# Kernel optimization log

Hardware: AMD Instinct MI355X
Metric: run time of the kernel (lower is better)

The kernel has to match this reference:

```python
import jax, jax.numpy as jnp
import numpy as np

N_HEAD = 16
N_EMBD = 64  # per-head dim in this module's convention
INNER = N_HEAD * N_EMBD  # 1024


def setup_inputs() -> dict:
    key = jax.random.key(0)
    ks = jax.random.split(key, 6)
    B, S = 4, 2048
    scale = 0.02
    return {
        "x": jax.random.normal(ks[0], (B, S, N_EMBD), dtype=jnp.float32),
        "Wq": jax.random.normal(ks[1], (N_EMBD, INNER), dtype=jnp.float32) * scale,
        "Wk": jax.random.normal(ks[2], (N_EMBD, INNER), dtype=jnp.float32) * scale,
        "Wv": jax.random.normal(ks[3], (N_EMBD, INNER), dtype=jnp.float32) * scale,
        "Wo": jax.random.normal(ks[4], (INNER, N_EMBD), dtype=jnp.float32) * scale,
        "bo": jax.random.normal(ks[5], (N_EMBD,), dtype=jnp.float32) * scale,
        "causal_mask": 1,
    }


def reference(x, Wq, Wk, Wv, Wo, bo, causal_mask):
    B, S, _ = x.shape
    # projections: [B,S,INNER] -> [B,H,S,D]
    def split_heads(t):
        return t.reshape(B, S, N_HEAD, N_EMBD).transpose(0, 2, 1, 3)
    q = split_heads(x @ Wq)
    k = split_heads(x @ Wk)
    v = split_heads(x @ Wv)
    # [B,H,S,S]
    scores = jnp.einsum("bhqd,bhkd->bhqk", q, k) / jnp.sqrt(jnp.float32(N_EMBD))
    if causal_mask:
        future = jnp.triu(jnp.ones((S, S), dtype=scores.dtype), k=1)
        scores = scores - 1e9 * future  # matches torch: subtract 1e9*mask
    attn = jax.nn.softmax(scores, axis=-1)
    out = jnp.einsum("bhqk,bhkd->bhqd", attn, v)
    out = out.transpose(0, 2, 1, 3).reshape(B, S, INNER)
    return out @ Wo + bo
```

## Files before the change

### kernel.cpp

```cpp
#include <hip/hip_runtime.h>
#include <hip/hip_bf16.h>

#define NHEAD 16
#define HDIM 64
#define DINNER 1024
#define NBATCH 4
#define SEQ 2048
#define NTOK (NBATCH*SEQ)

typedef __bf16 bf16;
typedef __bf16 bf16x4 __attribute__((ext_vector_type(4)));
typedef __bf16 bf16x8 __attribute__((ext_vector_type(8)));
typedef float f32x4 __attribute__((ext_vector_type(4)));

#define OFF_BO   8
#define OFF_XB   128
#define OFF_WQT  (OFF_XB + NTOK*HDIM)
#define OFF_WKT  (OFF_WQT + DINNER*HDIM)
#define OFF_WVT  (OFF_WKT + DINNER*HDIM)
#define OFF_WOT  (OFF_WVT + DINNER*HDIM)
#define OFF_Q    (OFF_WOT + DINNER*HDIM)
#define OFF_K    (OFF_Q + NTOK*DINNER)
#define OFF_VT   (OFF_K + NTOK*DINNER)
#define OFF_ATT  (OFF_VT + NTOK*DINNER)

#define SSCALE 0.18033688011112042f

static __device__ __forceinline__ bf16x8 ld8(const bf16* p) {
  return *reinterpret_cast<const bf16x8*>(p);
}

static __device__ __forceinline__ int detect_isbf(const void* x, int tid,
                                                  int* sflag) {
  if (tid < 64) {
    const unsigned short* xb = (const unsigned short*)x;
    bool ok = true;
#pragma unroll
    for (int i = 0; i < 8; i++) {
      unsigned e = (xb[tid * 8 + i] >> 7) & 0xFF;
      ok = ok && (e >= 64 && e <= 140);
    }
    unsigned long long mball = __ballot(ok);
    if (tid == 0) *sflag = (mball == ~0ull) ? 1 : 0;
  }
  __syncthreads();
  return *sflag;
}

__global__ __launch_bounds__(256) void prep_kernel(
    const void* __restrict__ x, const void* __restrict__ Wq,
    const void* __restrict__ Wk, const void* __restrict__ Wv,
    const void* __restrict__ Wo, const void* __restrict__ bo,
    bf16* __restrict__ ws) {
  __shared__ int sflag;
  int isbf = detect_isbf(x, threadIdx.x, &sflag);
  int z = blockIdx.y;
  int idx = blockIdx.x * 256 + threadIdx.x;
  if (z < 3) {
    const void* src = (z == 0) ? Wq : (z == 1) ? Wk : Wv;
    bf16* dst = ws + ((z == 0) ? OFF_WQT : (z == 1) ? OFF_WKT : OFF_WVT);
    int d = idx >> 10, n = idx & 1023;
    float v = isbf ? (float)((const bf16*)src)[idx] : ((const float*)src)[idx];
    if (z == 0) v *= SSCALE;
    dst[n * HDIM + d] = (bf16)v;
  } else if (z == 3) {
    int k = idx >> 6, n = idx & 63;
    float v = isbf ? (float)((const bf16*)Wo)[idx] : ((const float*)Wo)[idx];
    ws[OFF_WOT + n * DINNER + k] = (bf16)v;
  } else if (z == 4) {
    int i = idx * 8;
    bf16x8 v;
    if (isbf) {
      v = ld8((const bf16*)x + i);
    } else {
      f32x4 a = *reinterpret_cast<const f32x4*>((const float*)x + i);
      f32x4 b2 = *reinterpret_cast<const f32x4*>((const float*)x + i + 4);
#pragma unroll
      for (int j = 0; j < 4; j++) { v[j] = (bf16)a[j]; v[4 + j] = (bf16)b2[j]; }
    }
    *reinterpret_cast<bf16x8*>(&ws[OFF_XB + i]) = v;
  } else {
    if (idx < 64) ws[OFF_BO + idx] = isbf ? ((const bf16*)bo)[idx] : (bf16)((const float*)bo)[idx];
  }
}

__global__ __launch_bounds__(256) void qkv_kernel(bf16* __restrict__ ws) {
  __shared__ __align__(16) bf16 Vst[4][16 * 72];
  int tt = blockIdx.x, pz = blockIdx.z;
  int w = threadIdx.x >> 6;
  int nc = blockIdx.y * 4 + w;
  int lane = threadIdx.x & 63;
  int lq = lane & 15, quad = lane >> 4;
  const bf16* WT = ws + OFF_WQT + pz * (DINNER * HDIM);
  int n0 = nc * 64;
  bf16x8 w0[4], w1[4];
#pragma unroll
  for (int c = 0; c < 4; c++) {
    const bf16* wr = WT + (n0 + c * 16 + lq) * HDIM;
    w0[c] = ld8(wr + quad * 8);
    w1[c] = ld8(wr + 32 + quad * 8);
  }
  bf16* Qb = ws + OFF_Q;
  bf16* Kb = ws + OFF_K;
  bf16* VTb = ws + OFF_VT;
  bf16x8 ao0[4], ao1[4];
  if (pz == 2) {
    const bf16* WoT = ws + OFF_WOT;
#pragma unroll
    for (int c = 0; c < 4; c++) {
      const bf16* orow = WoT + (size_t)(c * 16 + lq) * DINNER + nc * 64;
      ao0[c] = ld8(orow + quad * 8);
      ao1[c] = ld8(orow + 32 + quad * 8);
    }
  }
#pragma unroll
  for (int mi = 0; mi < 4; mi++) {
    int t0 = tt * 64 + mi * 16;
    const bf16* xrow = ws + OFF_XB + (t0 + lq) * HDIM;
    bf16x8 x0 = ld8(xrow + quad * 8);
    bf16x8 x1 = ld8(xrow + 32 + quad * 8);
    int b = t0 >> 11, s0 = t0 & (SEQ - 1);
    if (pz < 2) {
#pragma unroll
      for (int c = 0; c < 4; c++) {
        f32x4 z = {0.f, 0.f, 0.f, 0.f};
        z = __builtin_amdgcn_mfma_f32_16x16x32_bf16(w0[c], x0, z, 0, 0, 0);
        z = __builtin_amdgcn_mfma_f32_16x16x32_bf16(w1[c], x1, z, 0, 0, 0);
        bf16x4 pk = {(bf16)z[0], (bf16)z[1], (bf16)z[2], (bf16)z[3]};
        bf16* P = (pz == 0) ? Qb : Kb;
        *reinterpret_cast<bf16x4*>(
            &P[((size_t)(b * NHEAD + nc) * SEQ + s0 + lq) * HDIM + c * 16 + quad * 4]) = pk;
      }
    } else {
#pragma unroll
      for (int c = 0; c < 4; c++) {
        f32x4 z = {0.f, 0.f, 0.f, 0.f};
        z = __builtin_amdgcn_mfma_f32_16x16x32_bf16(w0[c], x0, z, 0, 0, 0);
        z = __builtin_amdgcn_mfma_f32_16x16x32_bf16(w1[c], x1, z, 0, 0, 0);
        bf16x4 pk = {(bf16)z[0], (bf16)z[1], (bf16)z[2], (bf16)z[3]};
        *reinterpret_cast<bf16x4*>(&Vst[w][lq * 72 + c * 16 + quad * 4]) = pk;
      }
      bf16x8 bv0 = ld8(&Vst[w][lq * 72 + quad * 8]);
      bf16x8 bv1 = ld8(&Vst[w][lq * 72 + 32 + quad * 8]);
#pragma unroll
      for (int c = 0; c < 4; c++) {
        f32x4 z2 = {0.f, 0.f, 0.f, 0.f};
        z2 = __builtin_amdgcn_mfma_f32_16x16x32_bf16(ao0[c], bv0, z2, 0, 0, 0);
        z2 = __builtin_amdgcn_mfma_f32_16x16x32_bf16(ao1[c], bv1, z2, 0, 0, 0);
#pragma unroll
        for (int r = 0; r < 4; r++) {
          int d = c * 16 + quad * 4 + r;
          VTb[(((size_t)b * NHEAD + nc) * HDIM + d) * SEQ + s0 + lq] = (bf16)z2[r];
        }
      }
    }
  }
}

__global__ __launch_bounds__(256, 2) void flash_kernel(const int* __restrict__ cmask,
                                                       bf16* __restrict__ ws) {
  __shared__ __align__(16) bf16 Kl[2][64 * 64];
  __shared__ __align__(16) bf16 Vl[2][64 * 64];
  __shared__ __align__(16) bf16 Pl[4][16 * 64];
  const int qmap[16] = {15,13,11,9,0,2,4,6,14,12,10,8,1,3,5,7};
  int bid = blockIdx.x;
  int bh = (bid & 7) * 8 + ((bid >> 3) & 7);
  int qt = qmap[bid >> 6];
  int w = threadIdx.x >> 6;
  int lane = threadIdx.x & 63;
  int lq = lane & 15, quad = lane >> 4;
  int causal = cmask[0];
  const bf16* Q = ws + OFF_Q + (size_t)bh * SEQ * HDIM;
  const bf16* K = ws + OFF_K + (size_t)bh * SEQ * HDIM;
  const bf16* VT = ws + OFF_VT + (size_t)bh * HDIM * SEQ;
  int b = bh >> 4, h = bh & 15;
  bf16* ar = ws + OFF_ATT;
  int sr = threadIdx.x >> 2;
  int sg = (threadIdx.x & 3) * 16;
  int sc0 = (((threadIdx.x & 3) * 2) ^ (sr & 7)) << 3;
  int sc1 = (((threadIdx.x & 3) * 2 + 1) ^ (sr & 7)) << 3;
  int rq0 = (quad ^ (lq & 7)) << 3;
  int rq1 = ((4 + quad) ^ (lq & 7)) << 3;

  int qb = qt * 128;
  int qw = qb + w * 32;
  int T = (causal ? (qb + 128) : SEQ) / 64;

  bf16x8 bq[2][2];
#pragma unroll
  for (int m = 0; m < 2; m++) {
    const bf16* qrow = Q + (qw + m * 16 + lq) * HDIM;
    bq[m][0] = ld8(qrow + quad * 8);
    bq[m][1] = ld8(qrow + 32 + quad * 8);
  }
  f32x4 o[2][4];
  float lsum[2] = {0.f, 0.f};
#pragma unroll
  for (int m = 0; m < 2; m++)
#pragma unroll
    for (int c = 0; c < 4; c++) o[m][c] = (f32x4){0.f, 0.f, 0.f, 0.f};

  bf16x8 kst0 = ld8(K + sr * HDIM + sg);
  bf16x8 kst1 = ld8(K + sr * HDIM + sg + 8);
  bf16x8 vst0 = ld8(VT + sr * SEQ + sg);
  bf16x8 vst1 = ld8(VT + sr * SEQ + sg + 8);

  for (int ti = 0; ti < T; ti++) {
    int buf = ti & 1;
    int k0 = ti * 64;
    *reinterpret_cast<bf16x8*>(&Kl[buf][sr * 64 + sc0]) = kst0;
    *reinterpret_cast<bf16x8*>(&Kl[buf][sr * 64 + sc1]) = kst1;
    *reinterpret_cast<bf16x8*>(&Vl[buf][sr * 64 + sc0]) = vst0;
    *reinterpret_cast<bf16x8*>(&Vl[buf][sr * 64 + sc1]) = vst1;
    int kn = (ti + 1 < T) ? (k0 + 64) : k0;
    kst0 = ld8(K + (kn + sr) * HDIM + sg);
    kst1 = ld8(K + (kn + sr) * HDIM + sg + 8);
    vst0 = ld8(VT + sr * SEQ + kn + sg);
    vst1 = ld8(VT + sr * SEQ + kn + sg + 8);
    __syncthreads();
    f32x4 st[2][4];
#pragma unroll
    for (int t = 0; t < 4; t++) {
      bf16x8 a0 = ld8(&Kl[buf][(t * 16 + lq) * 64 + rq0]);
      bf16x8 a1 = ld8(&Kl[buf][(t * 16 + lq) * 64 + rq1]);
#pragma unroll
      for (int m = 0; m < 2; m++) {
        f32x4 z = {0.f, 0.f, 0.f, 0.f};
        z = __builtin_amdgcn_mfma_f32_16x16x32_bf16(a0, bq[m][0], z, 0, 0, 0);
        z = __builtin_amdgcn_mfma_f32_16x16x32_bf16(a1, bq[m][1], z, 0, 0, 0);
        st[m][t] = z;
      }
    }
    bool needmask = causal && (k0 + 63 > qw);
    bf16x8 bp[2][2];
#pragma unroll
    for (int m = 0; m < 2; m++) {
      if (needmask) {
        int qrel = qw + m * 16 + lq - k0 - quad * 4;
#pragma unroll
        for (int t = 0; t < 4; t++)
#pragma unroll
          for (int r = 0; r < 4; r++)
            if (t * 16 + r > qrel) st[m][t][r] = -200.0f;
      }
      float sum = 0.f;
#pragma unroll
      for (int t = 0; t < 4; t++) {
        float e0 = exp2f(st[m][t][0]);
        float e1 = exp2f(st[m][t][1]);
        float e2 = exp2f(st[m][t][2]);
        float e3 = exp2f(st[m][t][3]);
        sum += (e0 + e1) + (e2 + e3);
        bf16x4 pk = {(bf16)e0, (bf16)e1, (bf16)e2, (bf16)e3};
        int ch = ((t * 2 + (quad >> 1)) ^ (lq & 7)) << 3;
        *reinterpret_cast<bf16x4*>(&Pl[w][lq * 64 + ch + (quad & 1) * 4]) = pk;
      }
      lsum[m] += sum;
      bp[m][0] = ld8(&Pl[w][lq * 64 + rq0]);
      bp[m][1] = ld8(&Pl[w][lq * 64 + rq1]);
    }
#pragma unroll
    for (int c = 0; c < 4; c++) {
      bf16x8 av0 = ld8(&Vl[buf][(c * 16 + lq) * 64 + rq0]);
      bf16x8 av1 = ld8(&Vl[buf][(c * 16 + lq) * 64 + rq1]);
#pragma unroll
      for (int m = 0; m < 2; m++) {
        o[m][c] = __builtin_amdgcn_mfma_f32_16x16x32_bf16(av0, bp[m][0], o[m][c], 0, 0, 0);
        o[m][c] = __builtin_amdgcn_mfma_f32_16x16x32_bf16(av1, bp[m][1], o[m][c], 0, 0, 0);
      }
    }
  }
#pragma unroll
  for (int m = 0; m < 2; m++) {
    lsum[m] += __shfl_xor(lsum[m], 16);
    lsum[m] += __shfl_xor(lsum[m], 32);
    float inv = 1.0f / lsum[m];
    size_t rowoff = ((size_t)(b * SEQ + qw + m * 16 + lq)) * DINNER + h * HDIM;
#pragma unroll
    for (int c = 0; c < 4; c++) {
      bf16x4 ov = {(bf16)(o[m][c][0] * inv), (bf16)(o[m][c][1] * inv),
                   (bf16)(o[m][c][2] * inv), (bf16)(o[m][c][3] * inv)};
      *reinterpret_cast<bf16x4*>(&ar[rowoff + c * 16 + quad * 4]) = ov;
    }
  }
}

__global__ __launch_bounds__(256) void reduce_kernel(const bf16* __restrict__ ws,
                                                     const void* __restrict__ x,
                                                     void* __restrict__ outp) {
  __shared__ int sflag;
  int isbf = detect_isbf(x, threadIdx.x, &sflag);
  int idx = blockIdx.x * 256 + threadIdx.x;
  int t = idx >> 6, d = idx & 63;
  const bf16* ar = ws + OFF_ATT + (size_t)t * DINNER + d;
  float s = (float)ws[OFF_BO + d];
#pragma unroll
  for (int h = 0; h < 16; h++) s += (float)ar[h * 64];
  if (isbf) ((bf16*)outp)[idx] = (bf16)s;
  else      ((float*)outp)[idx] = s;
}

extern "C" void kernel_launch(void* const* d_in, const int* in_sizes, int n_in,
                              void* d_out, int out_size, void* d_ws, size_t ws_size,
                              hipStream_t stream) {
  const void* x  = d_in[0];
  const void* Wq = d_in[1];
  const void* Wk = d_in[2];
  const void* Wv = d_in[3];
  const void* Wo = d_in[4];
  const void* bo = d_in[5];
  const int* cm  = (const int*)d_in[6];
  bf16* ws = (bf16*)d_ws;

  hipLaunchKernelGGL(prep_kernel, dim3(256, 6), dim3(256), 0, stream,
                     x, Wq, Wk, Wv, Wo, bo, ws);
  hipLaunchKernelGGL(qkv_kernel, dim3(128, 4, 3), dim3(256), 0, stream, ws);
  hipLaunchKernelGGL(flash_kernel, dim3(1024), dim3(256), 0, stream, cm, ws);
  hipLaunchKernelGGL(reduce_kernel, dim3(2048), dim3(256), 0, stream, ws, x, d_out);
}
```

Measured before the change: 161.2 us.

## Fold input prep into QKV kernel and fuse head reduction into flash tail

Removes the separate prep kernel: the QKV kernel now reads and converts x and the weights directly from the inputs, with strided scalar loads for the transposed weight tiles. It also removes the reduce kernel: each flash block bumps an atomic counter per (batch, q-tile), and the last of the 16 head blocks sums the per-head outputs plus bias and writes the final result. This saves two launches and a workspace round trip, at the cost of uncoalesced weight loads repeated across every QKV block and a serialized tail in the last-arriving flash block. Correctness depends on the counters being zeroed by the QKV kernel before flash runs.

```diff
diff --git a/kernel.cpp b/kernel.cpp
--- a/kernel.cpp
+++ b/kernel.cpp
@@ -13,13 +13,7 @@
 typedef __bf16 bf16x8 __attribute__((ext_vector_type(8)));
 typedef float f32x4 __attribute__((ext_vector_type(4)));
 
-#define OFF_BO   8
-#define OFF_XB   128
-#define OFF_WQT  (OFF_XB + NTOK*HDIM)
-#define OFF_WKT  (OFF_WQT + DINNER*HDIM)
-#define OFF_WVT  (OFF_WKT + DINNER*HDIM)
-#define OFF_WOT  (OFF_WVT + DINNER*HDIM)
-#define OFF_Q    (OFF_WOT + DINNER*HDIM)
+#define OFF_Q    128
 #define OFF_K    (OFF_Q + NTOK*DINNER)
 #define OFF_VT   (OFF_K + NTOK*DINNER)
 #define OFF_ATT  (OFF_VT + NTOK*DINNER)
@@ -28,6 +22,9 @@
 
 static __device__ __forceinline__ bf16x8 ld8(const bf16* p) {
   return *reinterpret_cast<const bf16x8*>(p);
+}
+static __device__ __forceinline__ float ldw(const void* W, int i, int isbf) {
+  return isbf ? (float)((const bf16*)W)[i] : ((const float*)W)[i];
 }
 
 static __device__ __forceinline__ int detect_isbf(const void* x, int tid,
@@ -47,78 +44,71 @@
   return *sflag;
 }
 
-__global__ __launch_bounds__(256) void prep_kernel(
+__global__ __launch_bounds__(256) void qkv_kernel(
     const void* __restrict__ x, const void* __restrict__ Wq,
     const void* __restrict__ Wk, const void* __restrict__ Wv,
-    const void* __restrict__ Wo, const void* __restrict__ bo,
-    bf16* __restrict__ ws) {
+    const void* __restrict__ Wo, bf16* __restrict__ ws) {
+  __shared__ __align__(16) bf16 Vst[4][16 * 72];
   __shared__ int sflag;
   int isbf = detect_isbf(x, threadIdx.x, &sflag);
-  int z = blockIdx.y;
-  int idx = blockIdx.x * 256 + threadIdx.x;
-  if (z < 3) {
-    const void* src = (z == 0) ? Wq : (z == 1) ? Wk : Wv;
-    bf16* dst = ws + ((z == 0) ? OFF_WQT : (z == 1) ? OFF_WKT : OFF_WVT);
-    int d = idx >> 10, n = idx & 1023;
-    float v = isbf ? (float)((const bf16*)src)[idx] : ((const float*)src)[idx];
-    if (z == 0) v *= SSCALE;
-    dst[n * HDIM + d] = (bf16)v;
-  } else if (z == 3) {
-    int k = idx >> 6, n = idx & 63;
-    float v = isbf ? (float)((const bf16*)Wo)[idx] : ((const float*)Wo)[idx];
-    ws[OFF_WOT + n * DINNER + k] = (bf16)v;
-  } else if (z == 4) {
-    int i = idx * 8;
-    bf16x8 v;
-    if (isbf) {
-      v = ld8((const bf16*)x + i);
-    } else {
-      f32x4 a = *reinterpret_cast<const f32x4*>((const float*)x + i);
-      f32x4 b2 = *reinterpret_cast<const f32x4*>((const float*)x + i + 4);
-#pragma unroll
-      for (int j = 0; j < 4; j++) { v[j] = (bf16)a[j]; v[4 + j] = (bf16)b2[j]; }
-    }
-    *reinterpret_cast<bf16x8*>(&ws[OFF_XB + i]) = v;
-  } else {
-    if (idx < 64) ws[OFF_BO + idx] = isbf ? ((const bf16*)bo)[idx] : (bf16)((const float*)bo)[idx];
-  }
-}
-
-__global__ __launch_bounds__(256) void qkv_kernel(bf16* __restrict__ ws) {
-  __shared__ __align__(16) bf16 Vst[4][16 * 72];
   int tt = blockIdx.x, pz = blockIdx.z;
   int w = threadIdx.x >> 6;
   int nc = blockIdx.y * 4 + w;
   int lane = threadIdx.x & 63;
   int lq = lane & 15, quad = lane >> 4;
-  const bf16* WT = ws + OFF_WQT + pz * (DINNER * HDIM);
+  if (tt == 0 && pz == 0 && blockIdx.y == 0 && threadIdx.x < 64)
+    ((int*)ws)[threadIdx.x] = 0;
+  const void* W = (pz == 0) ? Wq : (pz == 1) ? Wk : Wv;
   int n0 = nc * 64;
   bf16x8 w0[4], w1[4];
 #pragma unroll
   for (int c = 0; c < 4; c++) {
-    const bf16* wr = WT + (n0 + c * 16 + lq) * HDIM;
-    w0[c] = ld8(wr + quad * 8);
-    w1[c] = ld8(wr + 32 + quad * 8);
+    int n = n0 + c * 16 + lq;
+#pragma unroll
+    for (int j = 0; j < 8; j++) {
+      float vA = ldw(W, (quad * 8 + j) * DINNER + n, isbf);
+      float vB = ldw(W, (32 + quad * 8 + j) * DINNER + n, isbf);
+      if (pz == 0) { vA *= SSCALE; vB *= SSCALE; }
+      w0[c][j] = (bf16)vA;
+      w1[c][j] = (bf16)vB;
+    }
+  }
+  bf16x8 ao0[4], ao1[4];
+  if (pz == 2) {
+#pragma unroll
+    for (int c = 0; c < 4; c++) {
+      int dout = c * 16 + lq;
+#pragma unroll
+      for (int j = 0; j < 8; j++) {
+        ao0[c][j] = (bf16)ldw(Wo, (n0 + quad * 8 + j) * HDIM + dout, isbf);
+        ao1[c][j] = (bf16)ldw(Wo, (n0 + 32 + quad * 8 + j) * HDIM + dout, isbf);
+      }
+    }
   }
   bf16* Qb = ws + OFF_Q;
   bf16* Kb = ws + OFF_K;
   bf16* VTb = ws + OFF_VT;
-  bf16x8 ao0[4], ao1[4];
-  if (pz == 2) {
-    const bf16* WoT = ws + OFF_WOT;
-#pragma unroll
-    for (int c = 0; c < 4; c++) {
-      const bf16* orow = WoT + (size_t)(c * 16 + lq) * DINNER + nc * 64;
-      ao0[c] = ld8(orow + quad * 8);
-      ao1[c] = ld8(orow + 32 + quad * 8);
-    }
-  }
 #pragma unroll
   for (int mi = 0; mi < 4; mi++) {
     int t0 = tt * 64 + mi * 16;
-    const bf16* xrow = ws + OFF_XB + (t0 + lq) * HDIM;
-    bf16x8 x0 = ld8(xrow + quad * 8);
-    bf16x8 x1 = ld8(xrow + 32 + quad * 8);
+    int trow = t0 + lq;
+    bf16x8 x0, x1;
+    if (isbf) {
+      const bf16* xr = (const bf16*)x + (size_t)trow * HDIM;
+      x0 = ld8(xr + quad * 8);
+      x1 = ld8(xr + 32 + quad * 8);
+    } else {
+      const float* xf = (const float*)x + (size_t)trow * HDIM;
+      f32x4 a0 = *reinterpret_cast<const f32x4*>(xf + quad * 8);
+      f32x4 a1 = *reinterpret_cast<const f32x4*>(xf + quad * 8 + 4);
+      f32x4 b0 = *reinterpret_cast<const f32x4*>(xf + 32 + quad * 8);
+      f32x4 b1 = *reinterpret_cast<const f32x4*>(xf + 32 + quad * 8 + 4);
+#pragma unroll
+      for (int j = 0; j < 4; j++) {
+        x0[j] = (bf16)a0[j]; x0[4 + j] = (bf16)a1[j];
+        x1[j] = (bf16)b0[j]; x1[4 + j] = (bf16)b1[j];
+      }
+    }
     int b = t0 >> 11, s0 = t0 & (SEQ - 1);
     if (pz < 2) {
 #pragma unroll
@@ -157,12 +147,17 @@
   }
 }
 
-__global__ __launch_bounds__(256, 2) void flash_kernel(const int* __restrict__ cmask,
-                                                       bf16* __restrict__ ws) {
+__global__ __launch_bounds__(256, 2) void flash_kernel(
+    const int* __restrict__ cmask, bf16* __restrict__ ws,
+    const void* __restrict__ x, const void* __restrict__ bo,
+    void* __restrict__ outp) {
   __shared__ __align__(16) bf16 Kl[2][64 * 64];
   __shared__ __align__(16) bf16 Vl[2][64 * 64];
   __shared__ __align__(16) bf16 Pl[4][16 * 64];
+  __shared__ int sflag;
+  __shared__ int isLast;
   const int qmap[16] = {15,13,11,9,0,2,4,6,14,12,10,8,1,3,5,7};
+  int isbf = detect_isbf(x, threadIdx.x, &sflag);
   int bid = blockIdx.x;
   int bh = (bid & 7) * 8 + ((bid >> 3) & 7);
   int qt = qmap[bid >> 6];
@@ -283,21 +278,27 @@
       *reinterpret_cast<bf16x4*>(&ar[rowoff + c * 16 + quad * 4]) = ov;
     }
   }
-}
-
-__global__ __launch_bounds__(256) void reduce_kernel(const bf16* __restrict__ ws,
-                                                     const void* __restrict__ x,
-                                                     void* __restrict__ outp) {
-  __shared__ int sflag;
-  int isbf = detect_isbf(x, threadIdx.x, &sflag);
-  int idx = blockIdx.x * 256 + threadIdx.x;
-  int t = idx >> 6, d = idx & 63;
-  const bf16* ar = ws + OFF_ATT + (size_t)t * DINNER + d;
-  float s = (float)ws[OFF_BO + d];
-#pragma unroll
-  for (int h = 0; h < 16; h++) s += (float)ar[h * 64];
-  if (isbf) ((bf16*)outp)[idx] = (bf16)s;
-  else      ((float*)outp)[idx] = s;
+  __threadfence();
+  if (threadIdx.x == 0) {
+    int old = atomicAdd(&((int*)ws)[b * 16 + qt], 1);
+    isLast = (old == 15);
+  }
+  __syncthreads();
+  if (isLast) {
+    __threadfence();
+#pragma unroll
+    for (int k = 0; k < 32; k++) {
+      int i = k * 256 + threadIdx.x;
+      int t = qb + (i >> 6), d = i & 63;
+      const bf16* arow = ws + OFF_ATT + ((size_t)(b * SEQ + t)) * DINNER + d;
+      float s = ldw(bo, d, isbf);
+#pragma unroll
+      for (int hh = 0; hh < 16; hh++) s += (float)arow[hh * 64];
+      size_t oo = (size_t)(b * SEQ + t) * HDIM + d;
+      if (isbf) ((bf16*)outp)[oo] = (bf16)s;
+      else      ((float*)outp)[oo] = s;
+    }
+  }
 }
 
 extern "C" void kernel_launch(void* const* d_in, const int* in_sizes, int n_in,
@@ -312,9 +313,8 @@
   const int* cm  = (const int*)d_in[6];
   bf16* ws = (bf16*)d_ws;
 
-  hipLaunchKernelGGL(prep_kernel, dim3(256, 6), dim3(256), 0, stream,
-                     x, Wq, Wk, Wv, Wo, bo, ws);
-  hipLaunchKernelGGL(qkv_kernel, dim3(128, 4, 3), dim3(256), 0, stream, ws);
-  hipLaunchKernelGGL(flash_kernel, dim3(1024), dim3(256), 0, stream, cm, ws);
-  hipLaunchKernelGGL(reduce_kernel, dim3(2048), dim3(256), 0, stream, ws, x, d_out);
-}
+  hipLaunchKernelGGL(qkv_kernel, dim3(128, 4, 3), dim3(256), 0, stream,
+                     x, Wq, Wk, Wv, Wo, ws);
+  hipLaunchKernelGGL(flash_kernel, dim3(1024), dim3(256), 0, stream,
+                     cm, ws, x, bo, d_out);
+}
```

Measured after the change: 320.1 us. 1.99x slower.

## Fuse Q/K/V projections into one block and read x directly

Applied to the files above, without the earlier changes.

The QKV projection kernel now computes Q, K and V (plus the Wo-folded V transform) in a single block, so each x tile is loaded once, where before each of three blocks loaded it. The bf16 staging copy of x in the prep kernel is removed and x is converted in registers inside the projection kernel, which also runs dtype detection. This cuts global traffic and one grid dimension, but raises per-thread register use from holding all four weight fragment sets at once, which may lower occupancy.

```diff
diff --git a/kernel.cpp b/kernel.cpp
--- a/kernel.cpp
+++ b/kernel.cpp
@@ -14,8 +14,7 @@
 typedef float f32x4 __attribute__((ext_vector_type(4)));
 
 #define OFF_BO   8
-#define OFF_XB   128
-#define OFF_WQT  (OFF_XB + NTOK*HDIM)
+#define OFF_WQT  128
 #define OFF_WKT  (OFF_WQT + DINNER*HDIM)
 #define OFF_WVT  (OFF_WKT + DINNER*HDIM)
 #define OFF_WOT  (OFF_WVT + DINNER*HDIM)
@@ -28,6 +27,9 @@
 
 static __device__ __forceinline__ bf16x8 ld8(const bf16* p) {
   return *reinterpret_cast<const bf16x8*>(p);
+}
+static __device__ __forceinline__ float ldw(const void* W, int i, int isbf) {
+  return isbf ? (float)((const bf16*)W)[i] : ((const float*)W)[i];
 }
 
 static __device__ __forceinline__ int detect_isbf(const void* x, int tid,
@@ -60,98 +62,99 @@
     const void* src = (z == 0) ? Wq : (z == 1) ? Wk : Wv;
     bf16* dst = ws + ((z == 0) ? OFF_WQT : (z == 1) ? OFF_WKT : OFF_WVT);
     int d = idx >> 10, n = idx & 1023;
-    float v = isbf ? (float)((const bf16*)src)[idx] : ((const float*)src)[idx];
+    float v = ldw(src, idx, isbf);
     if (z == 0) v *= SSCALE;
     dst[n * HDIM + d] = (bf16)v;
   } else if (z == 3) {
     int k = idx >> 6, n = idx & 63;
-    float v = isbf ? (float)((const bf16*)Wo)[idx] : ((const float*)Wo)[idx];
-    ws[OFF_WOT + n * DINNER + k] = (bf16)v;
-  } else if (z == 4) {
-    int i = idx * 8;
-    bf16x8 v;
-    if (isbf) {
-      v = ld8((const bf16*)x + i);
-    } else {
-      f32x4 a = *reinterpret_cast<const f32x4*>((const float*)x + i);
-      f32x4 b2 = *reinterpret_cast<const f32x4*>((const float*)x + i + 4);
-#pragma unroll
-      for (int j = 0; j < 4; j++) { v[j] = (bf16)a[j]; v[4 + j] = (bf16)b2[j]; }
-    }
-    *reinterpret_cast<bf16x8*>(&ws[OFF_XB + i]) = v;
+    ws[OFF_WOT + n * DINNER + k] = (bf16)ldw(Wo, idx, isbf);
   } else {
-    if (idx < 64) ws[OFF_BO + idx] = isbf ? ((const bf16*)bo)[idx] : (bf16)((const float*)bo)[idx];
-  }
-}
-
-__global__ __launch_bounds__(256) void qkv_kernel(bf16* __restrict__ ws) {
+    if (idx < 64) ws[OFF_BO + idx] = (bf16)ldw(bo, idx, isbf);
+  }
+}
+
+__global__ __launch_bounds__(256) void qkv_kernel(const void* __restrict__ x,
+                                                  bf16* __restrict__ ws) {
   __shared__ __align__(16) bf16 Vst[4][16 * 72];
-  int tt = blockIdx.x, pz = blockIdx.z;
+  __shared__ int sflag;
+  int isbf = detect_isbf(x, threadIdx.x, &sflag);
+  int tt = blockIdx.x;
   int w = threadIdx.x >> 6;
   int nc = blockIdx.y * 4 + w;
   int lane = threadIdx.x & 63;
   int lq = lane & 15, quad = lane >> 4;
-  const bf16* WT = ws + OFF_WQT + pz * (DINNER * HDIM);
   int n0 = nc * 64;
-  bf16x8 w0[4], w1[4];
+  bf16x8 wq0[4], wq1[4], wk0[4], wk1[4], wv0[4], wv1[4], ao0[4], ao1[4];
 #pragma unroll
   for (int c = 0; c < 4; c++) {
-    const bf16* wr = WT + (n0 + c * 16 + lq) * HDIM;
-    w0[c] = ld8(wr + quad * 8);
-    w1[c] = ld8(wr + 32 + quad * 8);
+    int n = n0 + c * 16 + lq;
+    const bf16* r;
+    r = ws + OFF_WQT + n * HDIM; wq0[c] = ld8(r + quad * 8); wq1[c] = ld8(r + 32 + quad * 8);
+    r = ws + OFF_WKT + n * HDIM; wk0[c] = ld8(r + quad * 8); wk1[c] = ld8(r + 32 + quad * 8);
+    r = ws + OFF_WVT + n * HDIM; wv0[c] = ld8(r + quad * 8); wv1[c] = ld8(r + 32 + quad * 8);
+    const bf16* orow = ws + OFF_WOT + (size_t)(c * 16 + lq) * DINNER + n0;
+    ao0[c] = ld8(orow + quad * 8); ao1[c] = ld8(orow + 32 + quad * 8);
   }
   bf16* Qb = ws + OFF_Q;
   bf16* Kb = ws + OFF_K;
   bf16* VTb = ws + OFF_VT;
-  bf16x8 ao0[4], ao1[4];
-  if (pz == 2) {
-    const bf16* WoT = ws + OFF_WOT;
-#pragma unroll
-    for (int c = 0; c < 4; c++) {
-      const bf16* orow = WoT + (size_t)(c * 16 + lq) * DINNER + nc * 64;
-      ao0[c] = ld8(orow + quad * 8);
-      ao1[c] = ld8(orow + 32 + quad * 8);
-    }
-  }
 #pragma unroll
   for (int mi = 0; mi < 4; mi++) {
     int t0 = tt * 64 + mi * 16;
-    const bf16* xrow = ws + OFF_XB + (t0 + lq) * HDIM;
-    bf16x8 x0 = ld8(xrow + quad * 8);
-    bf16x8 x1 = ld8(xrow + 32 + quad * 8);
+    bf16x8 x0, x1;
+    if (isbf) {
+      const bf16* xr = (const bf16*)x + (size_t)(t0 + lq) * HDIM;
+      x0 = ld8(xr + quad * 8);
+      x1 = ld8(xr + 32 + quad * 8);
+    } else {
+      const float* xf = (const float*)x + (size_t)(t0 + lq) * HDIM;
+      f32x4 a0 = *reinterpret_cast<const f32x4*>(xf + quad * 8);
+      f32x4 a1 = *reinterpret_cast<const f32x4*>(xf + quad * 8 + 4);
+      f32x4 b0 = *reinterpret_cast<const f32x4*>(xf + 32 + quad * 8);
+      f32x4 b1 = *reinterpret_cast<const f32x4*>(xf + 32 + quad * 8 + 4);
+#pragma unroll
+      for (int j = 0; j < 4; j++) {
+        x0[j] = (bf16)a0[j]; x0[4 + j] = (bf16)a1[j];
+        x1[j] = (bf16)b0[j]; x1[4 + j] = (bf16)b1[j];
+      }
+    }
     int b = t0 >> 11, s0 = t0 & (SEQ - 1);
-    if (pz < 2) {
-#pragma unroll
-      for (int c = 0; c < 4; c++) {
-        f32x4 z = {0.f, 0.f, 0.f, 0.f};
-        z = __builtin_amdgcn_mfma_f32_16x16x32_bf16(w0[c], x0, z, 0, 0, 0);
-        z = __builtin_amdgcn_mfma_f32_16x16x32_bf16(w1[c], x1, z, 0, 0, 0);
-        bf16x4 pk = {(bf16)z[0], (bf16)z[1], (bf16)z[2], (bf16)z[3]};
-        bf16* P = (pz == 0) ? Qb : Kb;
-        *reinterpret_cast<bf16x4*>(
-            &P[((size_t)(b * NHEAD + nc) * SEQ + s0 + lq) * HDIM + c * 16 + quad * 4]) = pk;
-      }
-    } else {
-#pragma unroll
-      for (int c = 0; c < 4; c++) {
-        f32x4 z = {0.f, 0.f, 0.f, 0.f};
-        z = __builtin_amdgcn_mfma_f32_16x16x32_bf16(w0[c], x0, z, 0, 0, 0);
-        z = __builtin_amdgcn_mfma_f32_16x16x32_bf16(w1[c], x1, z, 0, 0, 0);
-        bf16x4 pk = {(bf16)z[0], (bf16)z[1], (bf16)z[2], (bf16)z[3]};
-        *reinterpret_cast<bf16x4*>(&Vst[w][lq * 72 + c * 16 + quad * 4]) = pk;
-      }
-      bf16x8 bv0 = ld8(&Vst[w][lq * 72 + quad * 8]);
-      bf16x8 bv1 = ld8(&Vst[w][lq * 72 + 32 + quad * 8]);
-#pragma unroll
-      for (int c = 0; c < 4; c++) {
-        f32x4 z2 = {0.f, 0.f, 0.f, 0.f};
-        z2 = __builtin_amdgcn_mfma_f32_16x16x32_bf16(ao0[c], bv0, z2, 0, 0, 0);
-        z2 = __builtin_amdgcn_mfma_f32_16x16x32_bf16(ao1[c], bv1, z2, 0, 0, 0);
-#pragma unroll
-        for (int r = 0; r < 4; r++) {
-          int d = c * 16 + quad * 4 + r;
-          VTb[(((size_t)b * NHEAD + nc) * HDIM + d) * SEQ + s0 + lq] = (bf16)z2[r];
-        }
+    size_t rowbase = ((size_t)(b * NHEAD + nc) * SEQ + s0 + lq) * HDIM;
+#pragma unroll
+    for (int c = 0; c < 4; c++) {
+      f32x4 z = {0.f, 0.f, 0.f, 0.f};
+      z = __builtin_amdgcn_mfma_f32_16x16x32_bf16(wq0[c], x0, z, 0, 0, 0);
+      z = __builtin_amdgcn_mfma_f32_16x16x32_bf16(wq1[c], x1, z, 0, 0, 0);
+      bf16x4 pk = {(bf16)z[0], (bf16)z[1], (bf16)z[2], (bf16)z[3]};
+      *reinterpret_cast<bf16x4*>(&Qb[rowbase + c * 16 + quad * 4]) = pk;
+    }
+#pragma unroll
+    for (int c = 0; c < 4; c++) {
+      f32x4 z = {0.f, 0.f, 0.f, 0.f};
+      z = __builtin_amdgcn_mfma_f32_16x16x32_bf16(wk0[c], x0, z, 0, 0, 0);
+      z = __builtin_amdgcn_mfma_f32_16x16x32_bf16(wk1[c], x1, z, 0, 0, 0);
+      bf16x4 pk = {(bf16)z[0], (bf16)z[1], (bf16)z[2], (bf16)z[3]};
+      *reinterpret_cast<bf16x4*>(&Kb[rowbase + c * 16 + quad * 4]) = pk;
+    }
+#pragma unroll
+    for (int c = 0; c < 4; c++) {
+      f32x4 z = {0.f, 0.f, 0.f, 0.f};
+      z = __builtin_amdgcn_mfma_f32_16x16x32_bf16(wv0[c], x0, z, 0, 0, 0);
+      z = __builtin_amdgcn_mfma_f32_16x16x32_bf16(wv1[c], x1, z, 0, 0, 0);
+      bf16x4 pk = {(bf16)z[0], (bf16)z[1], (bf16)z[2], (bf16)z[3]};
+      *reinterpret_cast<bf16x4*>(&Vst[w][lq * 72 + c * 16 + quad * 4]) = pk;
+    }
+    bf16x8 bv0 = ld8(&Vst[w][lq * 72 + quad * 8]);
+    bf16x8 bv1 = ld8(&Vst[w][lq * 72 + 32 + quad * 8]);
+#pragma unroll
+    for (int c = 0; c < 4; c++) {
+      f32x4 z2 = {0.f, 0.f, 0.f, 0.f};
+      z2 = __builtin_amdgcn_mfma_f32_16x16x32_bf16(ao0[c], bv0, z2, 0, 0, 0);
+      z2 = __builtin_amdgcn_mfma_f32_16x16x32_bf16(ao1[c], bv1, z2, 0, 0, 0);
+#pragma unroll
+      for (int r = 0; r < 4; r++) {
+        int d = c * 16 + quad * 4 + r;
+        VTb[(((size_t)b * NHEAD + nc) * HDIM + d) * SEQ + s0 + lq] = (bf16)z2[r];
       }
     }
   }
@@ -312,9 +315,9 @@
   const int* cm  = (const int*)d_in[6];
   bf16* ws = (bf16*)d_ws;
 
-  hipLaunchKernelGGL(prep_kernel, dim3(256, 6), dim3(256), 0, stream,
+  hipLaunchKernelGGL(prep_kernel, dim3(256, 5), dim3(256), 0, stream,
                      x, Wq, Wk, Wv, Wo, bo, ws);
-  hipLaunchKernelGGL(qkv_kernel, dim3(128, 4, 3), dim3(256), 0, stream, ws);
+  hipLaunchKernelGGL(qkv_kernel, dim3(128, 4), dim3(256), 0, stream, x, ws);
   hipLaunchKernelGGL(flash_kernel, dim3(1024), dim3(256), 0, stream, cm, ws);
   hipLaunchKernelGGL(reduce_kernel, dim3(2048), dim3(256), 0, stream, ws, x, d_out);
 }
```

Measured after the change: 164.1 us. About the same (+1.8%).
